# Kernel optimization log

Hardware: AMD Instinct MI355X
Metric: run time of the kernel (lower is better)

The kernel has to match this reference:

```python
import jax, jax.numpy as jnp
import numpy as np

M_GROUP = 8  # VENOM m: pattern period along in_features

def _nm_mask(in_features, dtype):
    # NMVectorSparsifier.get_random_mask keeps positions 0 and 2 of every group of m=8
    pat = jnp.array([1.0, 0.0, 1.0, 0.0, 0.0, 0.0, 0.0, 0.0], dtype=dtype)
    return jnp.tile(pat, in_features // M_GROUP)  # [in_features]


def setup_inputs() -> dict:
    key = jax.random.key(0)
    k1, k2, k3 = jax.random.split(key, 3)
    B, S, D_IN, D_OUT = 8, 2048, 4096, 4096
    x = jax.random.normal(k1, (B, S, D_IN), dtype=jnp.float32)
    weight = jax.random.normal(k2, (D_OUT, D_IN), dtype=jnp.float32) * 0.02
    bias = jax.random.normal(k3, (D_OUT,), dtype=jnp.float32) * 0.02
    return {"x": x, "weight": weight, "bias": bias}


def reference(x, weight, bias):
    # y = x @ (W * mask)^T + b  -- N:M (2:8) vector-sparse linear, dense-math reference
    mask = _nm_mask(weight.shape[1], weight.dtype)  # [D_IN]
    w = weight * mask[None, :]                      # [D_OUT, D_IN]
    return jnp.einsum('bsd,od->bso', x, w) + bias
```

## Files before the change

kernel.cpp:

```cpp
#include <hip/hip_runtime.h>
#include <hip/hip_bf16.h>
#include <stdint.h>

#define MROWS 16384
#define DIN   4096
#define DOUT  4096
#define KEFF  1024

typedef __attribute__((ext_vector_type(8))) __bf16 bf16x8;
typedef __attribute__((ext_vector_type(4))) float f32x4;

__device__ __forceinline__ uint32_t f2bf_rne(float f) {
  union { float f; uint32_t u; } v; v.f = f;
  uint32_t u = v.u;
  return (u + 0x7fffu + ((u >> 16) & 1u)) >> 16;
}

__global__ void venom_gather(const float* __restrict__ src,
                             uint32_t* __restrict__ dst, int ngroups) {
  int stride = gridDim.x * blockDim.x;
  for (int i = blockIdx.x * blockDim.x + threadIdx.x; i < ngroups; i += stride) {
    const float4 v = *reinterpret_cast<const float4*>(src + (size_t)i * 8);
    dst[i] = f2bf_rne(v.x) | (f2bf_rne(v.z) << 16);
  }
}

#define BM 256
#define BN 256
#define BK 64
#define NT (KEFF / BK)

__global__ __launch_bounds__(512, 2) void venom_gemm(
    const __bf16* __restrict__ A, const __bf16* __restrict__ Bm,
    const float* __restrict__ bias, float* __restrict__ C) {
  __shared__ __bf16 As[2][BM * BK];
  __shared__ __bf16 Bs[2][BN * BK];

  const int nblkN = DOUT / BN;
  int nwg = gridDim.x;
  int cpx = nwg >> 3;
  int bid = blockIdx.x;
  int swz = (bid & 7) * cpx + (bid >> 3);
  int mblk = swz / nblkN;
  int nblk = swz % nblkN;

  int t = threadIdx.x;
  int wid = t >> 6, l = t & 63;
  int wr = wid >> 2, wc = wid & 3;
  int lr = l & 15, lg = l >> 4;
  int lswz = (l & 7) << 4;

  const __bf16* Ag = A + (size_t)(mblk * BM) * KEFF;
  const __bf16* Bg = Bm + (size_t)(nblk * BN) * KEFF;

  f32x4 acc[8][4] = {};

  auto stage = [&](int buf, int kt) {
    const int k0 = kt * BK;
    #pragma unroll
    for (int i = 0; i < 4; ++i) {
      int e = i * 512 + t;
      int row = e >> 3;
      int inL = ((e & 7) * 16) ^ ((row & 7) << 4);
      __builtin_amdgcn_global_load_lds(
          (const __attribute__((address_space(1))) uint32_t*)(Ag + (size_t)row * KEFF + k0 + (inL >> 1)),
          ((__attribute__((address_space(3))) uint32_t*)&As[buf][0]) + e * 4, 16, 0, 0);
    }
    #pragma unroll
    for (int i = 0; i < 4; ++i) {
      int e = i * 512 + t;
      int row = e >> 3;
      int inL = ((e & 7) * 16) ^ ((row & 7) << 4);
      __builtin_amdgcn_global_load_lds(
          (const __attribute__((address_space(1))) uint32_t*)(Bg + (size_t)row * KEFF + k0 + (inL >> 1)),
          ((__attribute__((address_space(3))) uint32_t*)&Bs[buf][0]) + e * 4, 16, 0, 0);
    }
  };

  stage(0, 0);
  asm volatile("s_waitcnt vmcnt(0)" ::: "memory");
  __builtin_amdgcn_s_barrier();

  bf16x8 bfrag[4];

  for (int kt = 0; kt < NT; ++kt) {
    int cur = kt & 1, nxt = cur ^ 1, t1 = kt + 1;
    const char* asBase = (const char*)&As[cur][0];
    const char* bsBase = (const char*)&Bs[cur][0];

    #pragma unroll
    for (int ph = 0; ph < 4; ++ph) {
      const int mh = ph & 1, kh = ph >> 1;
      const int kswz = (kh * 64 + lg * 16) ^ lswz;

      bf16x8 af[4];
      #pragma unroll
      for (int mi = 0; mi < 4; ++mi)
        af[mi] = *(const bf16x8*)(asBase +
                   (wr * 128 + mh * 64 + mi * 16 + lr) * 128 + kswz);
      if (mh == 0) {
        #pragma unroll
        for (int ni = 0; ni < 4; ++ni)
          bfrag[ni] = *(const bf16x8*)(bsBase +
                       (wc * 64 + ni * 16 + lr) * 128 + kswz);
      }
      if (ph == 0 && t1 < NT) stage(nxt, t1);

      __builtin_amdgcn_s_barrier();
      __builtin_amdgcn_s_setprio(1);
      #pragma unroll
      for (int mi = 0; mi < 4; ++mi)
        #pragma unroll
        for (int ni = 0; ni < 4; ++ni)
          acc[mh * 4 + mi][ni] = __builtin_amdgcn_mfma_f32_16x16x32_bf16(
              af[mi], bfrag[ni], acc[mh * 4 + mi][ni], 0, 0, 0);
      __builtin_amdgcn_s_setprio(0);
      if (ph < 3) __builtin_amdgcn_s_barrier();
    }

    if (t1 < NT) asm volatile("s_waitcnt vmcnt(0)" ::: "memory");
    __builtin_amdgcn_s_barrier();
  }

  int colbase = nblk * BN + wc * 64;
  int rowbase = mblk * BM + wr * 128;
  #pragma unroll
  for (int mh = 0; mh < 2; ++mh)
    #pragma unroll
    for (int mi = 0; mi < 4; ++mi) {
      int row0 = rowbase + mh * 64 + mi * 16 + lg * 4;
      #pragma unroll
      for (int ni = 0; ni < 4; ++ni) {
        int col = colbase + ni * 16 + lr;
        float bv = bias[col];
        f32x4 cv = acc[mh * 4 + mi][ni];
        #pragma unroll
        for (int j = 0; j < 4; ++j)
          C[(size_t)(row0 + j) * DOUT + col] = cv[j] + bv;
      }
    }
}

__global__ void venom_naive(const float* __restrict__ x, const float* __restrict__ w,
                            const float* __restrict__ bias, float* __restrict__ out) {
  size_t total = (size_t)MROWS * DOUT;
  size_t stride = (size_t)gridDim.x * blockDim.x;
  for (size_t idx = (size_t)blockIdx.x * blockDim.x + threadIdx.x; idx < total;
       idx += stride) {
    int m = (int)(idx / DOUT), n = (int)(idx % DOUT);
    const float* xr = x + (size_t)m * DIN;
    const float* wr = w + (size_t)n * DIN;
    float s = 0.f;
    for (int g = 0; g < DIN / 8; ++g)
      s += xr[g * 8] * wr[g * 8] + xr[g * 8 + 2] * wr[g * 8 + 2];
    out[idx] = s + bias[n];
  }
}

extern "C" void kernel_launch(void* const* d_in, const int* in_sizes, int n_in,
                              void* d_out, int out_size, void* d_ws, size_t ws_size,
                              hipStream_t stream) {
  const float* x    = (const float*)d_in[0];
  const float* wgt  = (const float*)d_in[1];
  const float* bias = (const float*)d_in[2];
  float* out = (float*)d_out;

  const size_t xg_bytes = (size_t)MROWS * KEFF * 2;
  const size_t wg_bytes = (size_t)DOUT * KEFF * 2;

  if (ws_size < xg_bytes + wg_bytes) {
    venom_naive<<<2048, 256, 0, stream>>>(x, wgt, bias, out);
    return;
  }

  uint32_t* xg = (uint32_t*)d_ws;
  uint32_t* wg = (uint32_t*)((char*)d_ws + xg_bytes);

  venom_gather<<<2048, 256, 0, stream>>>(x, xg, MROWS * (DIN / 8));
  venom_gather<<<512, 256, 0, stream>>>(wgt, wg, DOUT * (DIN / 8));

  venom_gemm<<<(MROWS / BM) * (DOUT / BN), 512, 0, stream>>>(
      (const __bf16*)xg, (const __bf16*)wg, bias, out);
}
```

Baseline: 289.8 us.

## Split K-tile staging into halves with partial vmcnt waits and new LDS swizzle

Each K tile of A and B is split into two 32-wide halves stored in separate LDS buffers. Each half is prefetched separately: the first half of the next tile is issued at phase 0 and the second at phase 2. Waits use s_waitcnt vmcnt(4) so compute on one half can start while loads for the other half are still in flight, which replaces the full vmcnt(0) drain at the end of every tile. A new row-pair XOR swizzle packs two rows per 128-byte LDS line to keep reads free of bank conflicts. The cost is more complex synchronisation that depends on exact outstanding-load counts.

```diff
diff --git a/kernel.cpp b/kernel.cpp
--- a/kernel.cpp
+++ b/kernel.cpp
@@ -9,6 +9,9 @@
 
 typedef __attribute__((ext_vector_type(8))) __bf16 bf16x8;
 typedef __attribute__((ext_vector_type(4))) float f32x4;
+
+#define AS1 __attribute__((address_space(1)))
+#define AS3 __attribute__((address_space(3)))
 
 __device__ __forceinline__ uint32_t f2bf_rne(float f) {
   union { float f; uint32_t u; } v; v.f = f;
@@ -30,11 +33,16 @@
 #define BK 64
 #define NT (KEFF / BK)
 
+__device__ __forceinline__ int swz_off(int R, int lg) {
+  int sr = R >> 1;
+  return sr * 128 + (((((R & 1) << 2) | lg) ^ (sr & 7)) << 4);
+}
+
 __global__ __launch_bounds__(512, 2) void venom_gemm(
     const __bf16* __restrict__ A, const __bf16* __restrict__ Bm,
     const float* __restrict__ bias, float* __restrict__ C) {
-  __shared__ __bf16 As[2][BM * BK];
-  __shared__ __bf16 Bs[2][BN * BK];
+  __shared__ __bf16 As[2][2][128 * 64];
+  __shared__ __bf16 Bs[2][2][128 * 64];
 
   const int nblkN = DOUT / BN;
   int nwg = gridDim.x;
@@ -48,63 +56,55 @@
   int wid = t >> 6, l = t & 63;
   int wr = wid >> 2, wc = wid & 3;
   int lr = l & 15, lg = l >> 4;
-  int lswz = (l & 7) << 4;
 
   const __bf16* Ag = A + (size_t)(mblk * BM) * KEFF;
   const __bf16* Bg = Bm + (size_t)(nblk * BN) * KEFF;
 
   f32x4 acc[8][4] = {};
 
-  auto stage = [&](int buf, int kt) {
-    const int k0 = kt * BK;
+  auto stage_half = [&](int buf, int kt, int kh) {
+    const int k0 = kt * BK + kh * 32;
     #pragma unroll
-    for (int i = 0; i < 4; ++i) {
+    for (int i = 0; i < 2; ++i) {
       int e = i * 512 + t;
-      int row = e >> 3;
-      int inL = ((e & 7) * 16) ^ ((row & 7) << 4);
+      int sr = e >> 3;
+      int s = (e & 7) ^ (sr & 7);
+      int row = sr * 2 + (s >> 2);
+      int koff = (s & 3) * 8;
       __builtin_amdgcn_global_load_lds(
-          (const __attribute__((address_space(1))) uint32_t*)(Ag + (size_t)row * KEFF + k0 + (inL >> 1)),
-          ((__attribute__((address_space(3))) uint32_t*)&As[buf][0]) + e * 4, 16, 0, 0);
-    }
-    #pragma unroll
-    for (int i = 0; i < 4; ++i) {
-      int e = i * 512 + t;
-      int row = e >> 3;
-      int inL = ((e & 7) * 16) ^ ((row & 7) << 4);
+          (const AS1 uint32_t*)(Ag + (size_t)row * KEFF + k0 + koff),
+          ((AS3 uint32_t*)&As[buf][kh][0]) + e * 4, 16, 0, 0);
       __builtin_amdgcn_global_load_lds(
-          (const __attribute__((address_space(1))) uint32_t*)(Bg + (size_t)row * KEFF + k0 + (inL >> 1)),
-          ((__attribute__((address_space(3))) uint32_t*)&Bs[buf][0]) + e * 4, 16, 0, 0);
+          (const AS1 uint32_t*)(Bg + (size_t)row * KEFF + k0 + koff),
+          ((AS3 uint32_t*)&Bs[buf][kh][0]) + e * 4, 16, 0, 0);
     }
   };
 
-  stage(0, 0);
-  asm volatile("s_waitcnt vmcnt(0)" ::: "memory");
+  stage_half(0, 0, 0);
+  stage_half(0, 0, 1);
+  asm volatile("s_waitcnt vmcnt(4)" ::: "memory");
   __builtin_amdgcn_s_barrier();
 
   bf16x8 bfrag[4];
 
   for (int kt = 0; kt < NT; ++kt) {
-    int cur = kt & 1, nxt = cur ^ 1, t1 = kt + 1;
-    const char* asBase = (const char*)&As[cur][0];
-    const char* bsBase = (const char*)&Bs[cur][0];
+    const int cur = kt & 1, nxt = cur ^ 1, t1 = kt + 1;
 
     #pragma unroll
     for (int ph = 0; ph < 4; ++ph) {
       const int mh = ph & 1, kh = ph >> 1;
-      const int kswz = (kh * 64 + lg * 16) ^ lswz;
-
+      const char* aB = (const char*)&As[cur][kh][0];
       bf16x8 af[4];
       #pragma unroll
       for (int mi = 0; mi < 4; ++mi)
-        af[mi] = *(const bf16x8*)(asBase +
-                   (wr * 128 + mh * 64 + mi * 16 + lr) * 128 + kswz);
+        af[mi] = *(const bf16x8*)(aB + swz_off(wr * 128 + mh * 64 + mi * 16 + lr, lg));
       if (mh == 0) {
+        const char* bB = (const char*)&Bs[cur][kh][0];
         #pragma unroll
         for (int ni = 0; ni < 4; ++ni)
-          bfrag[ni] = *(const bf16x8*)(bsBase +
-                       (wc * 64 + ni * 16 + lr) * 128 + kswz);
+          bfrag[ni] = *(const bf16x8*)(bB + swz_off(wc * 64 + ni * 16 + lr, lg));
+        if (t1 < NT) stage_half(nxt, t1, kh);
       }
-      if (ph == 0 && t1 < NT) stage(nxt, t1);
 
       __builtin_amdgcn_s_barrier();
       __builtin_amdgcn_s_setprio(1);
@@ -115,11 +115,20 @@
           acc[mh * 4 + mi][ni] = __builtin_amdgcn_mfma_f32_16x16x32_bf16(
               af[mi], bfrag[ni], acc[mh * 4 + mi][ni], 0, 0, 0);
       __builtin_amdgcn_s_setprio(0);
-      if (ph < 3) __builtin_amdgcn_s_barrier();
+
+      if (ph == 1) {
+        if (t1 < NT) asm volatile("s_waitcnt vmcnt(4)" ::: "memory");
+        else         asm volatile("s_waitcnt vmcnt(0)" ::: "memory");
+        __builtin_amdgcn_s_barrier();
+      } else if (ph == 3) {
+        if (t1 < NT) {
+          asm volatile("s_waitcnt vmcnt(4)" ::: "memory");
+          __builtin_amdgcn_s_barrier();
+        }
+      } else {
+        __builtin_amdgcn_s_barrier();
+      }
     }
-
-    if (t1 < NT) asm volatile("s_waitcnt vmcnt(0)" ::: "memory");
-    __builtin_amdgcn_s_barrier();
   }
 
   int colbase = nblk * BN + wc * 64;
```

Result: slower. 301.2 us (+3.9%).
